# Performance work log

Measured on AMD Instinct MI355X. Metric: run time of the kernel, lower is better.

## Reference

```python
import jax, jax.numpy as jnp
import numpy as np

N_E = 8192
E_DIM = 256
BETA = 0.25


def setup_inputs() -> dict:
    key = jax.random.key(0)
    k1, k2 = jax.random.split(key)
    z = jax.random.normal(k1, (16, E_DIM, 32, 32), dtype=jnp.float32)
    # matches torch init: uniform(-1/n_e, 1/n_e)
    emb_w = jax.random.uniform(k2, (N_E, E_DIM), dtype=jnp.float32,
                               minval=-1.0 / N_E, maxval=1.0 / N_E)
    return {"z": z, "emb_w": emb_w}


def reference(z, emb_w):
    B, C, H, W = z.shape
    zt = jnp.transpose(z, (0, 2, 3, 1))          # b h w c
    zf = zt.reshape(-1, C)                        # [N, e_dim]
    # d[n, k] = ||zf_n||^2 + ||e_k||^2 - 2 zf_n . e_k
    d = (jnp.sum(zf * zf, axis=1, keepdims=True)
         + jnp.sum(emb_w * emb_w, axis=1)
         - 2.0 * jnp.einsum('bd,nd->bn', zf, emb_w))
    idx = jnp.argmin(d, axis=1)                   # [N]
    z_q = emb_w[idx].reshape(zt.shape)            # b h w c
    sg = jax.lax.stop_gradient
    # legacy=True loss
    loss = jnp.mean((sg(z_q) - zt) ** 2) + BETA * jnp.mean((z_q - sg(zt)) ** 2)
    # straight-through estimator
    z_q_st = zt + sg(z_q - zt)
    z_q_out = jnp.transpose(z_q_st, (0, 3, 1, 2))  # b c h w
    return z_q_out, loss, idx.reshape(B, H, W)
```

## Files before the change

kernel.cpp:

```cpp
#include <hip/hip_runtime.h>
#include <math.h>

typedef unsigned int uint;
typedef unsigned short ushort;
typedef unsigned long long u64;
typedef __attribute__((ext_vector_type(8))) short short8;
typedef __attribute__((ext_vector_type(4))) float f32x4;

#define WS_ZT   0ull
#define WS_ZPK  16777216ull
#define WS_EPK  25165824ull
#define WS_SUMZ 29360128ull
#define WS_GMAX 29425664ull
#define WS_BEST 62980096ull
#define WS_LOSS 63111168ull

#define DOT_MARGIN 1.5e-4f

__device__ __forceinline__ ushort f2bf(float f) {
  uint b = __float_as_uint(f);
  b += 0x7fffu + ((b >> 16) & 1u);
  return (ushort)(b >> 16);
}
__device__ __forceinline__ uint ford(float f) {
  uint b = __float_as_uint(f);
  return (b & 0x80000000u) ? ~b : (b | 0x80000000u);
}
__device__ __forceinline__ void gload_lds16(const void* g, void* l) {
  __builtin_amdgcn_global_load_lds(
      (const __attribute__((address_space(1))) unsigned int*)g,
      (__attribute__((address_space(3))) unsigned int*)l, 16, 0, 0);
}

__global__ __launch_bounds__(256) void prep_all(const float* __restrict__ z,
                                                const float* __restrict__ emb,
                                                float* __restrict__ zt,
                                                ushort* __restrict__ zpk,
                                                ushort* __restrict__ epk,
                                                float* __restrict__ sumz) {
  __shared__ float tile[64][65];
  const int bidg = blockIdx.x;
  const int t = threadIdx.x;
  if (bidg < 1024) {
    const int bid = bidg;
    const int kt = bid & 3, hwt = (bid >> 2) & 15, b = bid >> 6;
    const int lane = t & 63, grp = t >> 6;
    const float* src = z + b * 262144 + (kt * 64) * 1024 + hwt * 64;
    for (int kk = grp; kk < 64; kk += 4)
      tile[kk][lane] = src[kk * 1024 + lane];
    __syncthreads();
    for (int rr = grp; rr < 64; rr += 4) {
      const int n = b * 1024 + hwt * 64 + rr;
      zt[n * 256 + kt * 64 + lane] = tile[lane][rr];
    }
    for (int u = t; u < 512; u += 256) {
      const int n_loc = u & 63, kg = u >> 6;
      const int n = b * 1024 + hwt * 64 + n_loc;
      const int k0 = kt * 64 + kg * 8;
      short8 s;
#pragma unroll
      for (int j = 0; j < 8; ++j) s[j] = (short)f2bf(tile[kg * 8 + j][n_loc]);
      *(short8*)(zpk + (size_t)(n >> 4) * 4096 + (k0 >> 5) * 512 +
                 ((k0 >> 3) & 3) * 128 + (n & 15) * 8) = s;
    }
  } else if (bidg < 2048) {
    const int u = (bidg - 1024) * 256 + t;
    const int c = u >> 5, k0 = (u & 31) * 8;
    const float4 v0 = *(const float4*)(emb + c * 256 + k0);
    const float4 v1 = *(const float4*)(emb + c * 256 + k0 + 4);
    short8 s;
    s[0] = (short)f2bf(v0.x); s[1] = (short)f2bf(v0.y);
    s[2] = (short)f2bf(v0.z); s[3] = (short)f2bf(v0.w);
    s[4] = (short)f2bf(v1.x); s[5] = (short)f2bf(v1.y);
    s[6] = (short)f2bf(v1.z); s[7] = (short)f2bf(v1.w);
    *(short8*)(epk + (size_t)(c >> 4) * 4096 + (k0 >> 5) * 512 +
               ((k0 >> 3) & 3) * 128 + (c & 15) * 8) = s;
  } else {
    const int n = ((bidg - 2048) << 8) + t;
    const int b = n >> 10, hw = n & 1023;
    const float* zb = z + b * 262144 + hw;
    float s = 0.f;
#pragma unroll 8
    for (int c = 0; c < 256; ++c) { const float v = zb[c << 10]; s += v * v; }
    sumz[n] = s;
  }
}

__global__ __launch_bounds__(256) void gemm_screen(const ushort* __restrict__ zpk,
                                                   const ushort* __restrict__ epk,
                                                   uint* __restrict__ gmax,
                                                   int boff) {
  __shared__ ushort Cs[16384];
  const int t = threadIdx.x;
  const int w = t >> 6, lane = t & 63;
  const int bid = blockIdx.x + boff;
  const int x = bid & 7, y = bid >> 3;
  const int colb = (y & 15) * 8 + x;
  const int rowg = y >> 4;
  const int n0 = rowg << 10;
  const int m16 = lane & 15, q = lane >> 4;
  const int cix = x * 64 + (y & 15) * 4 + q;

#pragma unroll
  for (int f2 = 0; f2 < 8; ++f2) {
    const int f = w * 8 + f2;
    gload_lds16(epk + (size_t)colb * 16384 + f * 512 + lane * 8, (char*)Cs + f * 1024);
  }

  const ushort* zw = zpk + ((size_t)(n0 >> 4) + w * 4) * 4096 + lane * 8;

  short8 zf[32][4];
#pragma unroll
  for (int v = 0; v < 3; ++v)
#pragma unroll
    for (int jr = 0; jr < 4; ++jr)
      zf[v][jr] = *(const short8*)(zw + ((size_t)((v >> 3) * 16 + jr)) * 4096 +
                                   (v & 7) * 512);
  __syncthreads();

#pragma unroll
  for (int strip = 0; strip < 4; ++strip) {
    const int rbase = n0 + strip * 256 + w * 64;
    f32x4 acc[4][4];
#pragma unroll
    for (int i = 0; i < 4; ++i)
#pragma unroll
      for (int j = 0; j < 4; ++j) acc[i][j] = {0.f, 0.f, 0.f, 0.f};

#pragma unroll
    for (int s32 = 0; s32 < 8; ++s32) {
      const int v = strip * 8 + s32;
      if (v + 3 < 32) {
        const int u = v + 3;
#pragma unroll
        for (int jr = 0; jr < 4; ++jr)
          zf[u][jr] = *(const short8*)(zw + ((size_t)((u >> 3) * 16 + jr)) * 4096 +
                                       (u & 7) * 512);
      }
      short8 cv[4];
#pragma unroll
      for (int ic = 0; ic < 4; ++ic)
        cv[ic] = *(const short8*)&Cs[(size_t)(ic * 8 + s32) * 512 + lane * 8];
#pragma unroll
      for (int ic = 0; ic < 4; ++ic)
#pragma unroll
        for (int jr = 0; jr < 4; ++jr)
          acc[ic][jr] = __builtin_amdgcn_mfma_f32_16x16x32_bf16(cv[ic], zf[v][jr],
                                                                acc[ic][jr], 0, 0, 0);
    }

#pragma unroll
    for (int jr = 0; jr < 4; ++jr) {
      uint pk[4];
#pragma unroll
      for (int ic = 0; ic < 4; ++ic) {
        float m = fmaxf(fmaxf(acc[ic][jr][0], acc[ic][jr][1]),
                        fmaxf(acc[ic][jr][2], acc[ic][jr][3]));
        m = fmaxf(m, __shfl_xor(m, 16, 64));
        const float o = __shfl_xor(m, 32, 64);
        const float glo = (q & 2) ? o : m;
        const float ghi = (q & 2) ? m : o;
        pk[ic] = (uint)f2bf(glo) | ((uint)f2bf(ghi) << 16);
      }
      const uint sv = (q == 0) ? pk[0] : (q == 1) ? pk[1] : (q == 2) ? pk[2] : pk[3];
      gmax[(size_t)(rbase + jr * 16 + m16) * 512 + cix] = sv;
    }
  }
}

__global__ __launch_bounds__(256) void select_rescore(const uint* __restrict__ gmax,
                                                      const float* __restrict__ zt,
                                                      const float* __restrict__ emb,
                                                      const float* __restrict__ sumz,
                                                      u64* __restrict__ best) {
  const int t = threadIdx.x, w = t >> 6, lane = t & 63;
  const int n = (blockIdx.x << 2) + w;
  __shared__ float zrow[4][256];
  __shared__ ushort hits[4][128];
  ((float4*)zrow[w])[lane] = ((const float4*)(zt + (size_t)n * 256))[lane];
  const uint4 r0 = ((const uint4*)(gmax + (size_t)n * 512))[lane];
  const uint4 r1 = ((const uint4*)(gmax + (size_t)n * 512))[lane + 64];
  const uint uv[8] = {r0.x, r0.y, r0.z, r0.w, r1.x, r1.y, r1.z, r1.w};
  float m = -INFINITY;
#pragma unroll
  for (int j = 0; j < 8; ++j) {
    m = fmaxf(m, __uint_as_float(uv[j] << 16));
    m = fmaxf(m, __uint_as_float(uv[j] & 0xffff0000u));
  }
#pragma unroll
  for (int off = 1; off < 64; off <<= 1) m = fmaxf(m, __shfl_xor(m, off, 64));
  const float thr = m - DOT_MARGIN;
  const u64 below = (1ull << lane) - 1ull;
  int base = 0;
#pragma unroll
  for (int j = 0; j < 8; ++j) {
    const int ui = (j < 4) ? lane * 4 + j : 256 + lane * 4 + (j - 4);
    {
      const bool hit = __uint_as_float(uv[j] << 16) >= thr;
      const u64 msk = __ballot(hit);
      if (hit) {
        const int p = base + (int)__popcll(msk & below);
        if (p < 128) hits[w][p] = (ushort)(ui * 2);
      }
      base += (int)__popcll(msk);
    }
    {
      const bool hit = __uint_as_float(uv[j] & 0xffff0000u) >= thr;
      const u64 msk = __ballot(hit);
      if (hit) {
        const int p = base + (int)__popcll(msk & below);
        if (p < 128) hits[w][p] = (ushort)(ui * 2 + 1);
      }
      base += (int)__popcll(msk);
    }
  }
  __threadfence_block();
  int K = base > 128 ? 128 : base;
  const float sz = sumz[n];
  u64 bk = ~0ull;
  for (int id = lane; id < K * 8; id += 64) {
    const int gid = hits[w][id >> 3];
    const int ci = gid >> 1, h = gid & 1;
    const int c = ((ci >> 2) & 15) * 512 + (ci >> 6) * 64 + (ci & 3) * 16 +
                  h * 8 + (id & 7);
    const float4* ea = (const float4*)(emb + c * 256);
    const float4* za = (const float4*)zrow[w];
    float sdot = 0.f, se = 0.f;
#pragma unroll 8
    for (int k = 0; k < 64; ++k) {
      const float4 a = za[k], e = ea[k];
      sdot = fmaf(a.x, e.x, sdot); sdot = fmaf(a.y, e.y, sdot);
      sdot = fmaf(a.z, e.z, sdot); sdot = fmaf(a.w, e.w, sdot);
      se = fmaf(e.x, e.x, se); se = fmaf(e.y, e.y, se);
      se = fmaf(e.z, e.z, se); se = fmaf(e.w, e.w, se);
    }
    const float d = (sz + se) - 2.f * sdot;
    const u64 key = ((u64)ford(d) << 32) | (uint)c;
    if (key < bk) bk = key;
  }
#pragma unroll
  for (int off = 1; off < 64; off <<= 1) {
    const u64 o = (((u64)(uint)__shfl_xor((int)(bk >> 32), off, 64)) << 32) |
                  (uint)__shfl_xor((int)(bk & 0xffffffffu), off, 64);
    if (o < bk) bk = o;
  }
  if (lane == 0) best[n] = bk;
}

__global__ __launch_bounds__(256) void gather_kernel(const float* __restrict__ z,
                                                     const float* __restrict__ emb,
                                                     const u64* __restrict__ best,
                                                     float* __restrict__ out,
                                                     double* __restrict__ loss_acc,
                                                     uint* __restrict__ done) {
  const int t = threadIdx.x;
  const int n0 = blockIdx.x << 6;
  const int n = n0 + (t & 63);
  const int idx = (int)(best[n] & 0xffffffffull);
  const int b_i = n >> 10, hw = n & 1023;
  const int c0 = t >> 6;
  const float* zb = z + b_i * 262144 + hw;
  float* ob = out + b_i * 262144 + hw;
  const float* eb = emb + idx * 256;
  float lsum = 0.f;
#pragma unroll 4
  for (int c = c0; c < 256; c += 4) {
    const float ev = eb[c];
    const float zv = zb[c << 10];
    ob[c << 10] = ev;
    const float d = ev - zv;
    lsum += d * d;
  }
  if (c0 == 0) out[4194305 + n] = (float)idx;
#pragma unroll
  for (int off = 32; off; off >>= 1) lsum += __shfl_down(lsum, off, 64);
  __shared__ double wsum[4];
  if ((t & 63) == 0) wsum[t >> 6] = (double)lsum;
  __syncthreads();
  if (t == 0) {
    atomicAdd(loss_acc, wsum[0] + wsum[1] + wsum[2] + wsum[3]);
    __threadfence();
    if (atomicAdd(done, 1u) == 255u) {
      __threadfence();
      out[4194304] = (float)(1.25 * (*(volatile double*)loss_acc) / 4194304.0);
    }
  }
}

extern "C" void kernel_launch(void* const* d_in, const int* in_sizes, int n_in,
                              void* d_out, int out_size, void* d_ws, size_t ws_size,
                              hipStream_t stream) {
  const float* z = (const float*)d_in[0];
  const float* emb = (const float*)d_in[1];
  float* out = (float*)d_out;
  char* ws = (char*)d_ws;
  float* zt = (float*)(ws + WS_ZT);
  ushort* zpk = (ushort*)(ws + WS_ZPK);
  ushort* epk = (ushort*)(ws + WS_EPK);
  float* sumz = (float*)(ws + WS_SUMZ);
  uint* gmax = (uint*)(ws + WS_GMAX);
  u64* best = (u64*)(ws + WS_BEST);
  double* loss_acc = (double*)(ws + WS_LOSS);
  uint* done = (uint*)(ws + WS_LOSS + 8);

  hipMemsetAsync(ws + WS_LOSS, 0, 16, stream);
  prep_all<<<2112, 256, 0, stream>>>(z, emb, zt, zpk, epk, sumz);
  gemm_screen<<<1024, 256, 0, stream>>>(zpk, epk, gmax, 0);
  gemm_screen<<<1024, 256, 0, stream>>>(zpk, epk, gmax, 1024);
  select_rescore<<<4096, 256, 0, stream>>>(gmax, zt, emb, sumz, best);
  gather_kernel<<<256, 256, 0, stream>>>(z, emb, best, out, loss_acc, done);
}
```

Baseline: 234.9 us.

## Use two-level hierarchical max screening with coarser 16-code groups

The GEMM screen now writes per-row maxima over 16-code groups plus a coarser per-64-code max, replacing the 8-code group maxima. The select kernel reads only the coarse 128-entry max array, picks coarse groups above threshold, then reads fine maxima only for those, and rescores up to 32 groups of 16 codes in fp32. This halves the screen output written and read, and cuts the selection ballot work. In exchange each hit group rescores 16 codes instead of 8, and the candidate cap changes, which could drop true minima when many groups pass the threshold.

```diff
diff --git a/kernel.cpp b/kernel.cpp
--- a/kernel.cpp
+++ b/kernel.cpp
@@ -12,8 +12,9 @@
 #define WS_EPK  25165824ull
 #define WS_SUMZ 29360128ull
 #define WS_GMAX 29425664ull
-#define WS_BEST 62980096ull
-#define WS_LOSS 63111168ull
+#define WS_CMAX 46202880ull
+#define WS_BEST 50397184ull
+#define WS_LOSS 50528256ull
 
 #define DOT_MARGIN 1.5e-4f
 
@@ -88,18 +89,19 @@
 
 __global__ __launch_bounds__(256) void gemm_screen(const ushort* __restrict__ zpk,
                                                    const ushort* __restrict__ epk,
-                                                   uint* __restrict__ gmax,
+                                                   uint* __restrict__ gmax16,
+                                                   ushort* __restrict__ cmax,
                                                    int boff) {
   __shared__ ushort Cs[16384];
   const int t = threadIdx.x;
   const int w = t >> 6, lane = t & 63;
   const int bid = blockIdx.x + boff;
   const int x = bid & 7, y = bid >> 3;
-  const int colb = (y & 15) * 8 + x;
+  const int yyv = y & 15;
+  const int colb = yyv * 8 + x;
   const int rowg = y >> 4;
   const int n0 = rowg << 10;
   const int m16 = lane & 15, q = lane >> 4;
-  const int cix = x * 64 + (y & 15) * 4 + q;
 
 #pragma unroll
   for (int f2 = 0; f2 < 8; ++f2) {
@@ -151,24 +153,31 @@
 
 #pragma unroll
     for (int jr = 0; jr < 4; ++jr) {
-      uint pk[4];
+      float g16[4];
+      float pm = -INFINITY;
 #pragma unroll
       for (int ic = 0; ic < 4; ++ic) {
         float m = fmaxf(fmaxf(acc[ic][jr][0], acc[ic][jr][1]),
                         fmaxf(acc[ic][jr][2], acc[ic][jr][3]));
         m = fmaxf(m, __shfl_xor(m, 16, 64));
         const float o = __shfl_xor(m, 32, 64);
-        const float glo = (q & 2) ? o : m;
-        const float ghi = (q & 2) ? m : o;
-        pk[ic] = (uint)f2bf(glo) | ((uint)f2bf(ghi) << 16);
+        const float g = fmaxf(m, o);
+        g16[ic] = g;
+        pm = fmaxf(pm, g);
       }
-      const uint sv = (q == 0) ? pk[0] : (q == 1) ? pk[1] : (q == 2) ? pk[2] : pk[3];
-      gmax[(size_t)(rbase + jr * 16 + m16) * 512 + cix] = sv;
-    }
-  }
-}
-
-__global__ __launch_bounds__(256) void select_rescore(const uint* __restrict__ gmax,
+      const int row = rbase + jr * 16 + m16;
+      const uint pa = (uint)f2bf(g16[0]) | ((uint)f2bf(g16[1]) << 16);
+      const uint pb = (uint)f2bf(g16[2]) | ((uint)f2bf(g16[3]) << 16);
+      if (q < 2)
+        gmax16[(size_t)row * 256 + x * 32 + yyv * 2 + q] = (q == 0) ? pa : pb;
+      if (q == 2)
+        cmax[(size_t)row * 128 + x * 16 + yyv] = f2bf(pm);
+    }
+  }
+}
+
+__global__ __launch_bounds__(256) void select_rescore(const uint* __restrict__ gmax16,
+                                                      const ushort* __restrict__ cmax,
                                                       const float* __restrict__ zt,
                                                       const float* __restrict__ emb,
                                                       const float* __restrict__ sumz,
@@ -176,53 +185,44 @@
   const int t = threadIdx.x, w = t >> 6, lane = t & 63;
   const int n = (blockIdx.x << 2) + w;
   __shared__ float zrow[4][256];
-  __shared__ ushort hits[4][128];
+  __shared__ ushort cands[4][32];
   ((float4*)zrow[w])[lane] = ((const float4*)(zt + (size_t)n * 256))[lane];
-  const uint4 r0 = ((const uint4*)(gmax + (size_t)n * 512))[lane];
-  const uint4 r1 = ((const uint4*)(gmax + (size_t)n * 512))[lane + 64];
-  const uint uv[8] = {r0.x, r0.y, r0.z, r0.w, r1.x, r1.y, r1.z, r1.w};
-  float m = -INFINITY;
-#pragma unroll
-  for (int j = 0; j < 8; ++j) {
-    m = fmaxf(m, __uint_as_float(uv[j] << 16));
-    m = fmaxf(m, __uint_as_float(uv[j] & 0xffff0000u));
-  }
+
+  const uint cu = ((const uint*)cmax)[(size_t)n * 64 + lane];
+  const float c0 = __uint_as_float(cu << 16);
+  const float c1 = __uint_as_float(cu & 0xffff0000u);
+  float m = fmaxf(c0, c1);
 #pragma unroll
   for (int off = 1; off < 64; off <<= 1) m = fmaxf(m, __shfl_xor(m, off, 64));
   const float thr = m - DOT_MARGIN;
-  const u64 below = (1ull << lane) - 1ull;
-  int base = 0;
-#pragma unroll
-  for (int j = 0; j < 8; ++j) {
-    const int ui = (j < 4) ? lane * 4 + j : 256 + lane * 4 + (j - 4);
-    {
-      const bool hit = __uint_as_float(uv[j] << 16) >= thr;
-      const u64 msk = __ballot(hit);
-      if (hit) {
-        const int p = base + (int)__popcll(msk & below);
-        if (p < 128) hits[w][p] = (ushort)(ui * 2);
-      }
-      base += (int)__popcll(msk);
-    }
-    {
-      const bool hit = __uint_as_float(uv[j] & 0xffff0000u) >= thr;
-      const u64 msk = __ballot(hit);
-      if (hit) {
-        const int p = base + (int)__popcll(msk & below);
-        if (p < 128) hits[w][p] = (ushort)(ui * 2 + 1);
-      }
-      base += (int)__popcll(msk);
-    }
-  }
-  __threadfence_block();
-  int K = base > 128 ? 128 : base;
+
+  u64 m0 = __ballot(c0 >= thr);
+  u64 m1 = __ballot(c1 >= thr);
+  int nc = 0;
+  while (m0 | m1) {
+    int colp;
+    if (m0) { const int s = __ffsll(m0) - 1; m0 &= m0 - 1; colp = s * 2; }
+    else    { const int s = __ffsll(m1) - 1; m1 &= m1 - 1; colp = s * 2 + 1; }
+    const int xx = colp >> 4, yy = colp & 15;
+    const uint ua = gmax16[(size_t)n * 256 + xx * 32 + yy * 2];
+    const uint ub = gmax16[(size_t)n * 256 + xx * 32 + yy * 2 + 1];
+    const int gb = (yy * 8 + xx) * 4;
+    const float f0 = __uint_as_float(ua << 16);
+    const float f1 = __uint_as_float(ua & 0xffff0000u);
+    const float f2 = __uint_as_float(ub << 16);
+    const float f3 = __uint_as_float(ub & 0xffff0000u);
+    if (f0 >= thr && nc < 32) { cands[w][nc] = (ushort)(gb + 0); ++nc; }
+    if (f1 >= thr && nc < 32) { cands[w][nc] = (ushort)(gb + 1); ++nc; }
+    if (f2 >= thr && nc < 32) { cands[w][nc] = (ushort)(gb + 2); ++nc; }
+    if (f3 >= thr && nc < 32) { cands[w][nc] = (ushort)(gb + 3); ++nc; }
+  }
+
+  const int K = nc;
   const float sz = sumz[n];
   u64 bk = ~0ull;
-  for (int id = lane; id < K * 8; id += 64) {
-    const int gid = hits[w][id >> 3];
-    const int ci = gid >> 1, h = gid & 1;
-    const int c = ((ci >> 2) & 15) * 512 + (ci >> 6) * 64 + (ci & 3) * 16 +
-                  h * 8 + (id & 7);
+  for (int id = lane; id < K * 16; id += 64) {
+    const int g = cands[w][id >> 4];
+    const int c = (g >> 2) * 64 + (g & 3) * 16 + (id & 15);
     const float4* ea = (const float4*)(emb + c * 256);
     const float4* za = (const float4*)zrow[w];
     float sdot = 0.f, se = 0.f;
@@ -298,15 +298,16 @@
   ushort* zpk = (ushort*)(ws + WS_ZPK);
   ushort* epk = (ushort*)(ws + WS_EPK);
   float* sumz = (float*)(ws + WS_SUMZ);
-  uint* gmax = (uint*)(ws + WS_GMAX);
+  uint* gmax16 = (uint*)(ws + WS_GMAX);
+  ushort* cmax = (ushort*)(ws + WS_CMAX);
   u64* best = (u64*)(ws + WS_BEST);
   double* loss_acc = (double*)(ws + WS_LOSS);
   uint* done = (uint*)(ws + WS_LOSS + 8);
 
   hipMemsetAsync(ws + WS_LOSS, 0, 16, stream);
   prep_all<<<2112, 256, 0, stream>>>(z, emb, zt, zpk, epk, sumz);
-  gemm_screen<<<1024, 256, 0, stream>>>(zpk, epk, gmax, 0);
-  gemm_screen<<<1024, 256, 0, stream>>>(zpk, epk, gmax, 1024);
-  select_rescore<<<4096, 256, 0, stream>>>(gmax, zt, emb, sumz, best);
+  gemm_screen<<<1024, 256, 0, stream>>>(zpk, epk, gmax16, cmax, 0);
+  gemm_screen<<<1024, 256, 0, stream>>>(zpk, epk, gmax16, cmax, 1024);
+  select_rescore<<<4096, 256, 0, stream>>>(gmax16, cmax, zt, emb, sumz, best);
   gather_kernel<<<256, 256, 0, stream>>>(z, emb, best, out, loss_acc, done);
 }
```

Result: slower. 265.1 us (+12.8%).
